# Optimization experiments

Hardware: AMD Instinct MI355X
Metric: run time of the kernel (lower is better)

The kernel has to match this reference:

```python
import jax, jax.numpy as jnp
import numpy as np

H_IN, W_IN = 128, 128  # sensor grid; region=(1,1), stride=(1,1) -> one RF per pixel


def setup_inputs() -> dict:
    key = jax.random.key(0)
    k1, k2, k3, k4, k5, k6 = jax.random.split(key, 6)
    B, N, C, HID = 8, 2048, 16, 128
    s = 1.0 / np.sqrt(HID)
    features = jax.random.normal(k1, (B, N, C), dtype=jnp.float32)
    coords = jax.random.randint(k2, (B, N, 2), 0, 128, dtype=jnp.int32)  # (x, y)
    w_ih = jax.random.normal(k3, (4 * HID, C), dtype=jnp.float32) * s
    w_hh = jax.random.normal(k4, (4 * HID, HID), dtype=jnp.float32) * s
    b_ih = jax.random.normal(k5, (4 * HID,), dtype=jnp.float32) * s
    b_hh = jax.random.normal(k6, (4 * HID,), dtype=jnp.float32) * s
    return {"features": features, "coords": coords, "w_ih": w_ih,
            "w_hh": w_hh, "b_ih": b_ih, "b_hh": b_hh}


def reference(features, coords, w_ih, w_hh, b_ih, b_hh):
    """MatrixLSTM with 1x1 non-overlapping receptive fields.

    Events (time-ordered along axis 1) are routed to their pixel's RF; a shared
    LSTM is run over each RF's event sequence and the last output per RF is
    scattered into a dense [B, hidden, H, W] map (zeros where no events).
    Implemented as one lax.scan over events with per-RF (h, c) state.
    """
    B, N, C = features.shape
    HID = w_hh.shape[1]
    # coord2idx: raster order y * W + x  -> RF id per event, [B, N]
    rf = coords[:, :, 1].astype(jnp.int32) * W_IN + coords[:, :, 0].astype(jnp.int32)
    bidx = jnp.arange(B)
    bias = b_ih + b_hh

    def step(carry, inp):
        h_all, c_all = carry              # [B, num_rf, HID] each
        x_t, rf_t = inp                   # [B, C], [B]
        h_prev = h_all[bidx, rf_t]        # gather per-RF state, [B, HID]
        c_prev = c_all[bidx, rf_t]
        gates = x_t @ w_ih.T + h_prev @ w_hh.T + bias  # [B, 4*HID]
        i, f, g, o = jnp.split(gates, 4, axis=-1)       # torch LSTM gate order
        i = jax.nn.sigmoid(i)
        f = jax.nn.sigmoid(f)
        g = jnp.tanh(g)
        o = jax.nn.sigmoid(o)
        c_new = f * c_prev + i * g
        h_new = o * jnp.tanh(c_new)
        h_all = h_all.at[bidx, rf_t].set(h_new)        # scatter back
        c_all = c_all.at[bidx, rf_t].set(c_new)
        return (h_all, c_all), None

    h0 = jnp.zeros((B, H_IN * W_IN, HID), features.dtype)
    c0 = jnp.zeros_like(h0)
    (h_all, _), _ = jax.lax.scan(step, (h0, c0),
                                 (features.transpose(1, 0, 2), rf.T))
    # final h per RF == LSTM output at each RF's last event; zeros if no events
    return h_all.reshape(B, H_IN, W_IN, HID).transpose(0, 3, 1, 2)
```

## Files before the change

### kernel.cpp

```cpp
#include <hip/hip_runtime.h>
#include <hip/hip_bf16.h>
#include <math.h>

#define B 8
#define N 2048
#define C 16
#define HID 128
#define NRF 16384
#define MAXLEN 8
#define MAXCH 2048

typedef __attribute__((ext_vector_type(4))) float f32x4;

__device__ __forceinline__ float sigf(float x) { return 1.f / (1.f + expf(-x)); }

__global__ __launch_bounds__(1024) void k_pre(
    const int* __restrict__ coords, const float* __restrict__ w_ih,
    const float* __restrict__ w_hh, const float* __restrict__ b_ih,
    const float* __restrict__ b_hh, float* __restrict__ w_ih_T,
    float* __restrict__ w_hh_T, float* __restrict__ biassum,
    int* __restrict__ map, int* __restrict__ cnt, int* __restrict__ mcnt,
    int* __restrict__ chainpk, int* __restrict__ mlist,
    int* __restrict__ slots) {
    int tid = threadIdx.x;
    if (blockIdx.x < 8) {
        int bb = blockIdx.x;
        __shared__ int cnt_l[NRF];
        __shared__ int nch_l, nmul_l;
#pragma unroll
        for (int i = 0; i < 16; i++) cnt_l[tid + 1024 * i] = 0;
        if (tid == 0) { nch_l = 0; nmul_l = 0; }
#pragma unroll
        for (int i = 0; i < 16; i++) map[bb * NRF + tid + 1024 * i] = -1;
        __syncthreads();
        int n0 = tid, n1 = tid + 1024;
        int2 c0 = ((const int2*)coords)[bb * N + n0];
        int2 c1 = ((const int2*)coords)[bb * N + n1];
        int rf0 = c0.y * 128 + c0.x;
        int rf1 = c1.y * 128 + c1.x;
        int pos0 = atomicAdd(&cnt_l[rf0], 1);
        int pos1 = atomicAdd(&cnt_l[rf1], 1);
        if (pos0 < MAXLEN) slots[((size_t)bb * NRF + rf0) * MAXLEN + pos0] = n0;
        if (pos1 < MAXLEN) slots[((size_t)bb * NRF + rf1) * MAXLEN + pos1] = n1;
        __syncthreads();
#pragma unroll
        for (int e = 0; e < 2; e++) {
            int rf = e ? rf1 : rf0;
            int pos = e ? pos1 : pos0;
            if (pos == 0) {
                int j = atomicAdd(&nch_l, 1);
                int len = cnt_l[rf];
                if (len > MAXLEN) len = MAXLEN;
                map[bb * NRF + rf] = j;
                int* sl = slots + ((size_t)bb * NRF + rf) * MAXLEN;
                int ev[MAXLEN];
#pragma unroll
                for (int t = 0; t < MAXLEN; t++) {
                    int v = sl[t];
                    ev[t] = (t < len) ? v : 0x7fffffff;
                }
#pragma unroll
                for (int a = 0; a < MAXLEN; a++)
#pragma unroll
                    for (int q = 0; q < MAXLEN - 1; q++) {
                        int u = ev[q], v = ev[q + 1];
                        ev[q] = min(u, v);
                        ev[q + 1] = max(u, v);
                    }
                if (len >= 2) {
                    for (int t = 0; t < len; t++) sl[t] = ev[t];
                    int m = atomicAdd(&nmul_l, 1);
                    if (m < 1024) mlist[bb * 1024 + m] = j | (rf << 11);
                }
                chainpk[bb * MAXCH + j] = ev[0] | (len << 11);
            }
        }
        __syncthreads();
        if (tid == 0) {
            cnt[bb] = nch_l;
            mcnt[bb] = (nmul_l > 1024) ? 1024 : nmul_l;
        }
    } else {
        int i = (blockIdx.x - 8) * 1024 + tid;
        if (i < C * 512) {
            int c = i >> 9, j = i & 511;
            w_ih_T[i] = w_ih[j * C + c];
        }
        if (i < HID * 512) {
            int k = i >> 9, j = i & 511;
            w_hh_T[i] = w_hh[j * HID + k];
        }
        if (i < 512) biassum[i] = b_ih[i] + b_hh[i];
    }
}

__global__ __launch_bounds__(512) void k_main(
    const float* __restrict__ features, const float* __restrict__ w_ih_T,
    const float* __restrict__ w_hh_T, const float* __restrict__ biassum,
    const int* __restrict__ cnt, const int* __restrict__ chainpk,
    const int* __restrict__ mcnt, const int* __restrict__ mlist,
    const int* __restrict__ slots, float* __restrict__ hfin) {
    int tid = threadIdx.x;
    __shared__ float ls_w[C * 512];
    __shared__ float ls_b[512];
    __shared__ int l_pk[16];
    __shared__ float h_s[HID], c_s[HID], x_s[16], g_s[512];

    if (blockIdx.x < 1024) {
        int bb = blockIdx.x >> 7;
        int m0 = blockIdx.x & 127;
        int M = mcnt[bb];
        if (m0 >= M) return;
        float wi[16];
#pragma unroll
        for (int c2 = 0; c2 < 16; c2++) wi[c2] = w_ih_T[c2 * 512 + tid];
        float bs = biassum[tid];
        for (int m = m0; m < M; m += 128) {
            int e = mlist[bb * 1024 + m];
            int j = e & 2047, rf = e >> 11;
            size_t idx = (size_t)(bb * MAXCH + j);
            int len = chainpk[bb * MAXCH + j] >> 11;
            const int* sl = slots + ((size_t)bb * NRF + rf) * MAXLEN;
            if (tid < 16) x_s[tid] = features[((size_t)(bb * N + sl[0])) * C + tid];
            if (tid < 128) c_s[tid] = 0.f;
            __syncthreads();
            for (int t = 0; t < len; t++) {
                float a0 = bs, a1 = 0.f, a2 = 0.f, a3 = 0.f;
#pragma unroll
                for (int c2 = 0; c2 < 16; c2++) a0 += wi[c2] * x_s[c2];
                if (t > 0) {
#pragma unroll 8
                    for (int k = 0; k < 128; k += 4) {
                        a0 += w_hh_T[k * 512 + tid]       * h_s[k];
                        a1 += w_hh_T[(k + 1) * 512 + tid] * h_s[k + 1];
                        a2 += w_hh_T[(k + 2) * 512 + tid] * h_s[k + 2];
                        a3 += w_hh_T[(k + 3) * 512 + tid] * h_s[k + 3];
                    }
                }
                g_s[tid] = (a0 + a1) + (a2 + a3);
                __syncthreads();
                if (tid < 128) {
                    float ig = sigf(g_s[tid]);
                    float fg = sigf(g_s[tid + 128]);
                    float gg = tanhf(g_s[tid + 256]);
                    float og = sigf(g_s[tid + 384]);
                    float cn = fg * c_s[tid] + ig * gg;
                    c_s[tid] = cn;
                    h_s[tid] = og * tanhf(cn);
                }
                if (tid < 16 && t + 1 < len)
                    x_s[tid] = features[((size_t)(bb * N + sl[t + 1])) * C + tid];
                __syncthreads();
            }
            if (tid < 128) hfin[idx * HID + tid] = h_s[tid];
            __syncthreads();
        }
    } else {
        int b2 = blockIdx.x - 1024;
        int bb = b2 >> 7;
        int slot0 = (b2 & 127) * 16;
        int nc = cnt[bb];
        if (tid < 16) {
            int j = slot0 + tid;
            l_pk[tid] = (j < nc) ? chainpk[bb * MAXCH + j] : -1;
        }
        for (int i = tid; i < C * 128; i += 512)
            ((float4*)ls_w)[i] = ((const float4*)w_ih_T)[i];
        ls_b[tid] = biassum[tid];
        __syncthreads();
        int w = tid >> 6, lane = tid & 63;
        int pk[2];
        float f[2];
#pragma unroll
        for (int s2 = 0; s2 < 2; s2++) {
            pk[s2] = l_pk[w * 2 + s2];
            f[s2] = 0.f;
            if (pk[s2] >= 0 && (pk[s2] >> 11) == 1 && lane < 16)
                f[s2] = features[((size_t)(bb * N + (pk[s2] & 2047))) * C + lane];
        }
#pragma unroll
        for (int s2 = 0; s2 < 2; s2++) {
            if (pk[s2] < 0 || (pk[s2] >> 11) != 1) continue;
            float ai0 = ls_b[lane],       ai1 = ls_b[lane + 64];
            float ag0 = ls_b[lane + 256], ag1 = ls_b[lane + 320];
            float ao0 = ls_b[lane + 384], ao1 = ls_b[lane + 448];
#pragma unroll
            for (int c2 = 0; c2 < 16; c2++) {
                float xv = __shfl(f[s2], c2, 64);
                ai0 += ls_w[c2 * 512 + lane]       * xv;
                ai1 += ls_w[c2 * 512 + lane + 64]  * xv;
                ag0 += ls_w[c2 * 512 + lane + 256] * xv;
                ag1 += ls_w[c2 * 512 + lane + 320] * xv;
                ao0 += ls_w[c2 * 512 + lane + 384] * xv;
                ao1 += ls_w[c2 * 512 + lane + 448] * xv;
            }
            float c0 = sigf(ai0) * tanhf(ag0);
            float c1 = sigf(ai1) * tanhf(ag1);
            float h0 = sigf(ao0) * tanhf(c0);
            float h1 = sigf(ao1) * tanhf(c1);
            size_t idx = (size_t)(bb * MAXCH + slot0 + w * 2 + s2);
            hfin[idx * HID + lane] = h0;
            hfin[idx * HID + lane + 64] = h1;
        }
    }
}

__global__ __launch_bounds__(256) void k_scatter(
    const float* __restrict__ hfin, const int* __restrict__ map,
    float* __restrict__ out) {
    int b = blockIdx.x >> 7;
    int y = blockIdx.x & 127;
    int t = threadIdx.x;
    int xq = t & 31;
    int hg = t >> 5;
    const int4* mrow = (const int4*)(map + b * NRF + y * 128);
    int4 kk = mrow[xq];
    const float* hb = hfin + (size_t)b * MAXCH * HID + hg * 16;
    float vx[16], vy[16], vz[16], vw[16];
#pragma unroll
    for (int q = 0; q < 4; q++) {
        float4 a = make_float4(0.f, 0.f, 0.f, 0.f);
        if (kk.x >= 0) a = *(const float4*)(hb + (size_t)kk.x * HID + q * 4);
        vx[q * 4 + 0] = a.x; vx[q * 4 + 1] = a.y;
        vx[q * 4 + 2] = a.z; vx[q * 4 + 3] = a.w;
    }
#pragma unroll
    for (int q = 0; q < 4; q++) {
        float4 a = make_float4(0.f, 0.f, 0.f, 0.f);
        if (kk.y >= 0) a = *(const float4*)(hb + (size_t)kk.y * HID + q * 4);
        vy[q * 4 + 0] = a.x; vy[q * 4 + 1] = a.y;
        vy[q * 4 + 2] = a.z; vy[q * 4 + 3] = a.w;
    }
#pragma unroll
    for (int q = 0; q < 4; q++) {
        float4 a = make_float4(0.f, 0.f, 0.f, 0.f);
        if (kk.z >= 0) a = *(const float4*)(hb + (size_t)kk.z * HID + q * 4);
        vz[q * 4 + 0] = a.x; vz[q * 4 + 1] = a.y;
        vz[q * 4 + 2] = a.z; vz[q * 4 + 3] = a.w;
    }
#pragma unroll
    for (int q = 0; q < 4; q++) {
        float4 a = make_float4(0.f, 0.f, 0.f, 0.f);
        if (kk.w >= 0) a = *(const float4*)(hb + (size_t)kk.w * HID + q * 4);
        vw[q * 4 + 0] = a.x; vw[q * 4 + 1] = a.y;
        vw[q * 4 + 2] = a.z; vw[q * 4 + 3] = a.w;
    }
#pragma unroll
    for (int hh = 0; hh < 16; hh++) {
        int hid = hg * 16 + hh;
        f32x4 v = {vx[hh], vy[hh], vz[hh], vw[hh]};
        __builtin_nontemporal_store(
            v, (f32x4*)(out + ((((size_t)b * HID + hid) * 128 + y) * 128) + xq * 4));
    }
}

extern "C" void kernel_launch(void* const* d_in, const int* in_sizes, int n_in,
                              void* d_out, int out_size, void* d_ws, size_t ws_size,
                              hipStream_t stream) {
    const float* features = (const float*)d_in[0];
    const int*   coords   = (const int*)d_in[1];
    const float* w_ih     = (const float*)d_in[2];
    const float* w_hh     = (const float*)d_in[3];
    const float* b_ih     = (const float*)d_in[4];
    const float* b_hh     = (const float*)d_in[5];
    float* out = (float*)d_out;

    char* ws = (char*)d_ws;
    float* w_ih_T   = (float*)(ws + 0);
    float* w_hh_T   = (float*)(ws + 32768);
    float* biassum  = (float*)(ws + 294912);
    int*   map      = (int*)(ws + 296960);
    int*   cnt      = (int*)(ws + 821248);
    int*   mcnt     = (int*)(ws + 821312);
    int*   chainpk  = (int*)(ws + 821376);
    int*   mlist    = (int*)(ws + 886912);
    int*   slots    = (int*)(ws + 919680);
    float* hfin     = (float*)(ws + 5113984);

    k_pre<<<dim3(81), dim3(1024), 0, stream>>>(
        coords, w_ih, w_hh, b_ih, b_hh, w_ih_T, w_hh_T, biassum,
        map, cnt, mcnt, chainpk, mlist, slots);
    k_main<<<dim3(2048), dim3(512), 0, stream>>>(
        features, w_ih_T, w_hh_T, biassum, cnt, chainpk, mcnt, mlist,
        slots, hfin);
    k_scatter<<<dim3(B * 128), dim3(256), 0, stream>>>(hfin, map, out);
}
```

Before: 131.4 us.

## Fuse preprocess, LSTM and scatter into one persistent kernel with grid barriers

Replaces the three separate launches with one 256-block persistent kernel. Two flag-based grid barriers with alternating magic values separate the preprocessing, LSTM and scatter phases. Each thread in the multi-event chain loop now keeps its full w_hh column (128 floats) in registers instead of re-reading it from global memory every step. Per-RF counters are packed as 16-bit halves in LDS so one 512-thread block can hold them, and the union shared layout lets phases reuse the same LDS. This removes launch gaps and repeated weight traffic, but it depends on all blocks being co-resident, adds heavy register pressure, and cuts the scatter and LSTM phases to fewer blocks.

```diff
diff --git a/kernel.cpp b/kernel.cpp
--- a/kernel.cpp
+++ b/kernel.cpp
@@ -1,5 +1,4 @@
 #include <hip/hip_runtime.h>
-#include <hip/hip_bf16.h>
 #include <math.h>
 
 #define B 8
@@ -9,50 +8,87 @@
 #define NRF 16384
 #define MAXLEN 8
 #define MAXCH 2048
+#define NBLK 256
+
+#define MAGIC1 0x1357BD13
+#define MAGIC2 0x2468ACE2
 
 typedef __attribute__((ext_vector_type(4))) float f32x4;
 
 __device__ __forceinline__ float sigf(float x) { return 1.f / (1.f + expf(-x)); }
 
-__global__ __launch_bounds__(1024) void k_pre(
-    const int* __restrict__ coords, const float* __restrict__ w_ih,
-    const float* __restrict__ w_hh, const float* __restrict__ b_ih,
-    const float* __restrict__ b_hh, float* __restrict__ w_ih_T,
-    float* __restrict__ w_hh_T, float* __restrict__ biassum,
-    int* __restrict__ map, int* __restrict__ cnt, int* __restrict__ mcnt,
+__device__ __forceinline__ void gridbar(int* flags, int magic) {
+    __syncthreads();
+    if (threadIdx.x == 0) {
+        __threadfence();
+        __hip_atomic_store(&flags[blockIdx.x], magic, __ATOMIC_RELEASE,
+                           __HIP_MEMORY_SCOPE_AGENT);
+    }
+    if (threadIdx.x < NBLK) {
+        while (__hip_atomic_load(&flags[threadIdx.x], __ATOMIC_ACQUIRE,
+                                 __HIP_MEMORY_SCOPE_AGENT) != magic)
+            __builtin_amdgcn_s_sleep(1);
+    }
+    __syncthreads();
+    __threadfence();
+}
+
+struct SmemPre {
+    unsigned int cnt16[NRF / 2];
+    int nch, nmul;
+};
+struct SmemMain {
+    float ls_w[C * 512];
+    float ls_b[512];
+    int   l_pk[64];
+    float h_s[HID], c_s[HID], x_s[16], g_s[512];
+};
+union Smem { SmemPre pre; SmemMain mn; };
+
+__global__ __launch_bounds__(512, 2) void k_all(
+    const float* __restrict__ features, const int* __restrict__ coords,
+    const float* __restrict__ w_ih, const float* __restrict__ w_hh,
+    const float* __restrict__ b_ih, const float* __restrict__ b_hh,
+    float* __restrict__ w_ih_T, float* __restrict__ w_hh_T,
+    float* __restrict__ biassum, int* __restrict__ map,
+    int* __restrict__ cnt, int* __restrict__ mcnt,
     int* __restrict__ chainpk, int* __restrict__ mlist,
-    int* __restrict__ slots) {
+    int* __restrict__ slots, float* __restrict__ hfin,
+    float* __restrict__ out, int* __restrict__ flags) {
+    __shared__ Smem sm;
     int tid = threadIdx.x;
-    if (blockIdx.x < 8) {
-        int bb = blockIdx.x;
-        __shared__ int cnt_l[NRF];
-        __shared__ int nch_l, nmul_l;
-#pragma unroll
-        for (int i = 0; i < 16; i++) cnt_l[tid + 1024 * i] = 0;
-        if (tid == 0) { nch_l = 0; nmul_l = 0; }
-#pragma unroll
-        for (int i = 0; i < 16; i++) map[bb * NRF + tid + 1024 * i] = -1;
+    int bid = blockIdx.x;
+
+    if (bid < 8) {
+        int bb = bid;
+#pragma unroll
+        for (int i = 0; i < 16; i++) sm.pre.cnt16[tid + 512 * i] = 0;
+        if (tid == 0) { sm.pre.nch = 0; sm.pre.nmul = 0; }
+#pragma unroll
+        for (int i = 0; i < 32; i++) map[bb * NRF + tid + 512 * i] = -1;
         __syncthreads();
-        int n0 = tid, n1 = tid + 1024;
-        int2 c0 = ((const int2*)coords)[bb * N + n0];
-        int2 c1 = ((const int2*)coords)[bb * N + n1];
-        int rf0 = c0.y * 128 + c0.x;
-        int rf1 = c1.y * 128 + c1.x;
-        int pos0 = atomicAdd(&cnt_l[rf0], 1);
-        int pos1 = atomicAdd(&cnt_l[rf1], 1);
-        if (pos0 < MAXLEN) slots[((size_t)bb * NRF + rf0) * MAXLEN + pos0] = n0;
-        if (pos1 < MAXLEN) slots[((size_t)bb * NRF + rf1) * MAXLEN + pos1] = n1;
+        int rf[4], pos[4];
+#pragma unroll
+        for (int e = 0; e < 4; e++) {
+            int n = tid + 512 * e;
+            int2 cc = ((const int2*)coords)[bb * N + n];
+            rf[e] = cc.y * 128 + cc.x;
+            int word = rf[e] >> 1, sh = (rf[e] & 1) << 4;
+            unsigned int old = atomicAdd(&sm.pre.cnt16[word], 1u << sh);
+            pos[e] = (int)((old >> sh) & 0xFFFFu);
+            if (pos[e] < MAXLEN)
+                slots[((size_t)bb * NRF + rf[e]) * MAXLEN + pos[e]] = n;
+        }
         __syncthreads();
 #pragma unroll
-        for (int e = 0; e < 2; e++) {
-            int rf = e ? rf1 : rf0;
-            int pos = e ? pos1 : pos0;
-            if (pos == 0) {
-                int j = atomicAdd(&nch_l, 1);
-                int len = cnt_l[rf];
+        for (int e = 0; e < 4; e++) {
+            if (pos[e] == 0) {
+                int j = atomicAdd(&sm.pre.nch, 1);
+                int word = rf[e] >> 1, sh = (rf[e] & 1) << 4;
+                int len = (int)((sm.pre.cnt16[word] >> sh) & 0xFFFFu);
                 if (len > MAXLEN) len = MAXLEN;
-                map[bb * NRF + rf] = j;
-                int* sl = slots + ((size_t)bb * NRF + rf) * MAXLEN;
+                map[bb * NRF + rf[e]] = j;
+                int* sl = slots + ((size_t)bb * NRF + rf[e]) * MAXLEN;
                 int ev[MAXLEN];
 #pragma unroll
                 for (int t = 0; t < MAXLEN; t++) {
@@ -69,22 +105,22 @@
                     }
                 if (len >= 2) {
                     for (int t = 0; t < len; t++) sl[t] = ev[t];
-                    int m = atomicAdd(&nmul_l, 1);
-                    if (m < 1024) mlist[bb * 1024 + m] = j | (rf << 11);
+                    int m = atomicAdd(&sm.pre.nmul, 1);
+                    if (m < 1024) mlist[bb * 1024 + m] = j | (rf[e] << 11);
                 }
                 chainpk[bb * MAXCH + j] = ev[0] | (len << 11);
             }
         }
         __syncthreads();
         if (tid == 0) {
-            cnt[bb] = nch_l;
-            mcnt[bb] = (nmul_l > 1024) ? 1024 : nmul_l;
+            cnt[bb] = sm.pre.nch;
+            mcnt[bb] = (sm.pre.nmul > 1024) ? 1024 : sm.pre.nmul;
         }
     } else {
-        int i = (blockIdx.x - 8) * 1024 + tid;
+        int i = (bid - 8) * 512 + tid;
         if (i < C * 512) {
-            int c = i >> 9, j = i & 511;
-            w_ih_T[i] = w_ih[j * C + c];
+            int c2 = i >> 9, j = i & 511;
+            w_ih_T[i] = w_ih[j * C + c2];
         }
         if (i < HID * 512) {
             int k = i >> 9, j = i & 511;
@@ -92,165 +128,152 @@
         }
         if (i < 512) biassum[i] = b_ih[i] + b_hh[i];
     }
-}
-
-__global__ __launch_bounds__(512) void k_main(
-    const float* __restrict__ features, const float* __restrict__ w_ih_T,
-    const float* __restrict__ w_hh_T, const float* __restrict__ biassum,
-    const int* __restrict__ cnt, const int* __restrict__ chainpk,
-    const int* __restrict__ mcnt, const int* __restrict__ mlist,
-    const int* __restrict__ slots, float* __restrict__ hfin) {
-    int tid = threadIdx.x;
-    __shared__ float ls_w[C * 512];
-    __shared__ float ls_b[512];
-    __shared__ int l_pk[16];
-    __shared__ float h_s[HID], c_s[HID], x_s[16], g_s[512];
-
-    if (blockIdx.x < 1024) {
-        int bb = blockIdx.x >> 7;
-        int m0 = blockIdx.x & 127;
+    gridbar(flags, MAGIC1);
+
+    {
+        for (int i = tid; i < C * 128; i += 512)
+            ((float4*)sm.mn.ls_w)[i] = ((const float4*)w_ih_T)[i];
+        sm.mn.ls_b[tid] = biassum[tid];
+        int gbb = bid >> 5;
+        int slot0 = (bid & 31) * 64;
+        if (tid < 64) {
+            int j = slot0 + tid;
+            sm.mn.l_pk[tid] = (j < cnt[gbb]) ? chainpk[gbb * MAXCH + j] : -1;
+        }
+
+        int bb = bid & 7, m0 = bid >> 3;
         int M = mcnt[bb];
-        if (m0 >= M) return;
+        float bs = biassum[tid];
         float wi[16];
-#pragma unroll
-        for (int c2 = 0; c2 < 16; c2++) wi[c2] = w_ih_T[c2 * 512 + tid];
-        float bs = biassum[tid];
-        for (int m = m0; m < M; m += 128) {
+        float wcol[128];
+        if (m0 < M) {
+#pragma unroll
+            for (int c2 = 0; c2 < 16; c2++) wi[c2] = w_ih_T[c2 * 512 + tid];
+#pragma unroll
+            for (int k = 0; k < 128; k++) wcol[k] = w_hh_T[k * 512 + tid];
+        }
+        for (int m = m0; m < M; m += 32) {
             int e = mlist[bb * 1024 + m];
             int j = e & 2047, rf = e >> 11;
             size_t idx = (size_t)(bb * MAXCH + j);
             int len = chainpk[bb * MAXCH + j] >> 11;
             const int* sl = slots + ((size_t)bb * NRF + rf) * MAXLEN;
-            if (tid < 16) x_s[tid] = features[((size_t)(bb * N + sl[0])) * C + tid];
-            if (tid < 128) c_s[tid] = 0.f;
+            if (tid < 16) sm.mn.x_s[tid] =
+                features[((size_t)(bb * N + sl[0])) * C + tid];
+            if (tid < 128) sm.mn.c_s[tid] = 0.f;
             __syncthreads();
             for (int t = 0; t < len; t++) {
                 float a0 = bs, a1 = 0.f, a2 = 0.f, a3 = 0.f;
 #pragma unroll
-                for (int c2 = 0; c2 < 16; c2++) a0 += wi[c2] * x_s[c2];
+                for (int c2 = 0; c2 < 16; c2++) a0 += wi[c2] * sm.mn.x_s[c2];
                 if (t > 0) {
-#pragma unroll 8
+#pragma unroll
                     for (int k = 0; k < 128; k += 4) {
-                        a0 += w_hh_T[k * 512 + tid]       * h_s[k];
-                        a1 += w_hh_T[(k + 1) * 512 + tid] * h_s[k + 1];
-                        a2 += w_hh_T[(k + 2) * 512 + tid] * h_s[k + 2];
-                        a3 += w_hh_T[(k + 3) * 512 + tid] * h_s[k + 3];
+                        a0 += wcol[k]     * sm.mn.h_s[k];
+                        a1 += wcol[k + 1] * sm.mn.h_s[k + 1];
+                        a2 += wcol[k + 2] * sm.mn.h_s[k + 2];
+                        a3 += wcol[k + 3] * sm.mn.h_s[k + 3];
                     }
                 }
-                g_s[tid] = (a0 + a1) + (a2 + a3);
+                sm.mn.g_s[tid] = (a0 + a1) + (a2 + a3);
                 __syncthreads();
                 if (tid < 128) {
-                    float ig = sigf(g_s[tid]);
-                    float fg = sigf(g_s[tid + 128]);
-                    float gg = tanhf(g_s[tid + 256]);
-                    float og = sigf(g_s[tid + 384]);
-                    float cn = fg * c_s[tid] + ig * gg;
-                    c_s[tid] = cn;
-                    h_s[tid] = og * tanhf(cn);
+                    float ig = sigf(sm.mn.g_s[tid]);
+                    float fg = sigf(sm.mn.g_s[tid + 128]);
+                    float gg = tanhf(sm.mn.g_s[tid + 256]);
+                    float og = sigf(sm.mn.g_s[tid + 384]);
+                    float cn = fg * sm.mn.c_s[tid] + ig * gg;
+                    sm.mn.c_s[tid] = cn;
+                    sm.mn.h_s[tid] = og * tanhf(cn);
                 }
                 if (tid < 16 && t + 1 < len)
-                    x_s[tid] = features[((size_t)(bb * N + sl[t + 1])) * C + tid];
+                    sm.mn.x_s[tid] =
+                        features[((size_t)(bb * N + sl[t + 1])) * C + tid];
                 __syncthreads();
             }
-            if (tid < 128) hfin[idx * HID + tid] = h_s[tid];
+            if (tid < 128) hfin[idx * HID + tid] = sm.mn.h_s[tid];
             __syncthreads();
         }
-    } else {
-        int b2 = blockIdx.x - 1024;
-        int bb = b2 >> 7;
-        int slot0 = (b2 & 127) * 16;
-        int nc = cnt[bb];
-        if (tid < 16) {
-            int j = slot0 + tid;
-            l_pk[tid] = (j < nc) ? chainpk[bb * MAXCH + j] : -1;
-        }
-        for (int i = tid; i < C * 128; i += 512)
-            ((float4*)ls_w)[i] = ((const float4*)w_ih_T)[i];
-        ls_b[tid] = biassum[tid];
         __syncthreads();
+
         int w = tid >> 6, lane = tid & 63;
-        int pk[2];
-        float f[2];
-#pragma unroll
-        for (int s2 = 0; s2 < 2; s2++) {
-            pk[s2] = l_pk[w * 2 + s2];
+        int pk[8];
+        float f[8];
+#pragma unroll
+        for (int s2 = 0; s2 < 8; s2++) {
+            pk[s2] = sm.mn.l_pk[w * 8 + s2];
             f[s2] = 0.f;
             if (pk[s2] >= 0 && (pk[s2] >> 11) == 1 && lane < 16)
-                f[s2] = features[((size_t)(bb * N + (pk[s2] & 2047))) * C + lane];
-        }
-#pragma unroll
-        for (int s2 = 0; s2 < 2; s2++) {
+                f[s2] = features[((size_t)(gbb * N + (pk[s2] & 2047))) * C + lane];
+        }
+#pragma unroll
+        for (int s2 = 0; s2 < 8; s2++) {
             if (pk[s2] < 0 || (pk[s2] >> 11) != 1) continue;
-            float ai0 = ls_b[lane],       ai1 = ls_b[lane + 64];
-            float ag0 = ls_b[lane + 256], ag1 = ls_b[lane + 320];
-            float ao0 = ls_b[lane + 384], ao1 = ls_b[lane + 448];
+            float ai0 = sm.mn.ls_b[lane],       ai1 = sm.mn.ls_b[lane + 64];
+            float ag0 = sm.mn.ls_b[lane + 256], ag1 = sm.mn.ls_b[lane + 320];
+            float ao0 = sm.mn.ls_b[lane + 384], ao1 = sm.mn.ls_b[lane + 448];
 #pragma unroll
             for (int c2 = 0; c2 < 16; c2++) {
                 float xv = __shfl(f[s2], c2, 64);
-                ai0 += ls_w[c2 * 512 + lane]       * xv;
-                ai1 += ls_w[c2 * 512 + lane + 64]  * xv;
-                ag0 += ls_w[c2 * 512 + lane + 256] * xv;
-                ag1 += ls_w[c2 * 512 + lane + 320] * xv;
-                ao0 += ls_w[c2 * 512 + lane + 384] * xv;
-                ao1 += ls_w[c2 * 512 + lane + 448] * xv;
-            }
-            float c0 = sigf(ai0) * tanhf(ag0);
-            float c1 = sigf(ai1) * tanhf(ag1);
-            float h0 = sigf(ao0) * tanhf(c0);
-            float h1 = sigf(ao1) * tanhf(c1);
-            size_t idx = (size_t)(bb * MAXCH + slot0 + w * 2 + s2);
+                ai0 += sm.mn.ls_w[c2 * 512 + lane]       * xv;
+                ai1 += sm.mn.ls_w[c2 * 512 + lane + 64]  * xv;
+                ag0 += sm.mn.ls_w[c2 * 512 + lane + 256] * xv;
+                ag1 += sm.mn.ls_w[c2 * 512 + lane + 320] * xv;
+                ao0 += sm.mn.ls_w[c2 * 512 + lane + 384] * xv;
+                ao1 += sm.mn.ls_w[c2 * 512 + lane + 448] * xv;
+            }
+            float cc0 = sigf(ai0) * tanhf(ag0);
+            float cc1 = sigf(ai1) * tanhf(ag1);
+            float h0 = sigf(ao0) * tanhf(cc0);
+            float h1 = sigf(ao1) * tanhf(cc1);
+            size_t idx = (size_t)(gbb * MAXCH + slot0 + w * 8 + s2);
             hfin[idx * HID + lane] = h0;
             hfin[idx * HID + lane + 64] = h1;
         }
     }
-}
-
-__global__ __launch_bounds__(256) void k_scatter(
-    const float* __restrict__ hfin, const int* __restrict__ map,
-    float* __restrict__ out) {
-    int b = blockIdx.x >> 7;
-    int y = blockIdx.x & 127;
-    int t = threadIdx.x;
-    int xq = t & 31;
-    int hg = t >> 5;
-    const int4* mrow = (const int4*)(map + b * NRF + y * 128);
-    int4 kk = mrow[xq];
-    const float* hb = hfin + (size_t)b * MAXCH * HID + hg * 16;
-    float vx[16], vy[16], vz[16], vw[16];
-#pragma unroll
-    for (int q = 0; q < 4; q++) {
-        float4 a = make_float4(0.f, 0.f, 0.f, 0.f);
-        if (kk.x >= 0) a = *(const float4*)(hb + (size_t)kk.x * HID + q * 4);
-        vx[q * 4 + 0] = a.x; vx[q * 4 + 1] = a.y;
-        vx[q * 4 + 2] = a.z; vx[q * 4 + 3] = a.w;
-    }
-#pragma unroll
-    for (int q = 0; q < 4; q++) {
-        float4 a = make_float4(0.f, 0.f, 0.f, 0.f);
-        if (kk.y >= 0) a = *(const float4*)(hb + (size_t)kk.y * HID + q * 4);
-        vy[q * 4 + 0] = a.x; vy[q * 4 + 1] = a.y;
-        vy[q * 4 + 2] = a.z; vy[q * 4 + 3] = a.w;
-    }
-#pragma unroll
-    for (int q = 0; q < 4; q++) {
-        float4 a = make_float4(0.f, 0.f, 0.f, 0.f);
-        if (kk.z >= 0) a = *(const float4*)(hb + (size_t)kk.z * HID + q * 4);
-        vz[q * 4 + 0] = a.x; vz[q * 4 + 1] = a.y;
-        vz[q * 4 + 2] = a.z; vz[q * 4 + 3] = a.w;
-    }
-#pragma unroll
-    for (int q = 0; q < 4; q++) {
-        float4 a = make_float4(0.f, 0.f, 0.f, 0.f);
-        if (kk.w >= 0) a = *(const float4*)(hb + (size_t)kk.w * HID + q * 4);
-        vw[q * 4 + 0] = a.x; vw[q * 4 + 1] = a.y;
-        vw[q * 4 + 2] = a.z; vw[q * 4 + 3] = a.w;
-    }
-#pragma unroll
-    for (int hh = 0; hh < 16; hh++) {
-        int hid = hg * 16 + hh;
-        f32x4 v = {vx[hh], vy[hh], vz[hh], vw[hh]};
-        __builtin_nontemporal_store(
-            v, (f32x4*)(out + ((((size_t)b * HID + hid) * 128 + y) * 128) + xq * 4));
+    gridbar(flags, MAGIC2);
+
+    {
+        int half = tid >> 8;
+        int t = tid & 255;
+        int xq = t & 31;
+        int hg = t >> 5;
+#pragma unroll
+        for (int p2 = 0; p2 < 2; p2++) {
+            int row = bid * 4 + p2 * 2 + half;
+            int b = row >> 7, y = row & 127;
+            const int4* mrow = (const int4*)(map + b * NRF + y * 128);
+            int4 kk = mrow[xq];
+            const float* hb = hfin + (size_t)b * MAXCH * HID + hg * 16;
+            float vx[16], vy[16], vz[16], vw[16];
+#pragma unroll
+            for (int q = 0; q < 4; q++) {
+                float4 a = make_float4(0.f, 0.f, 0.f, 0.f);
+                if (kk.x >= 0) a = *(const float4*)(hb + (size_t)kk.x * HID + q * 4);
+                vx[q * 4 + 0] = a.x; vx[q * 4 + 1] = a.y;
+                vx[q * 4 + 2] = a.z; vx[q * 4 + 3] = a.w;
+                a = make_float4(0.f, 0.f, 0.f, 0.f);
+                if (kk.y >= 0) a = *(const float4*)(hb + (size_t)kk.y * HID + q * 4);
+                vy[q * 4 + 0] = a.x; vy[q * 4 + 1] = a.y;
+                vy[q * 4 + 2] = a.z; vy[q * 4 + 3] = a.w;
+                a = make_float4(0.f, 0.f, 0.f, 0.f);
+                if (kk.z >= 0) a = *(const float4*)(hb + (size_t)kk.z * HID + q * 4);
+                vz[q * 4 + 0] = a.x; vz[q * 4 + 1] = a.y;
+                vz[q * 4 + 2] = a.z; vz[q * 4 + 3] = a.w;
+                a = make_float4(0.f, 0.f, 0.f, 0.f);
+                if (kk.w >= 0) a = *(const float4*)(hb + (size_t)kk.w * HID + q * 4);
+                vw[q * 4 + 0] = a.x; vw[q * 4 + 1] = a.y;
+                vw[q * 4 + 2] = a.z; vw[q * 4 + 3] = a.w;
+            }
+#pragma unroll
+            for (int hh = 0; hh < 16; hh++) {
+                int hid = hg * 16 + hh;
+                f32x4 v = {vx[hh], vy[hh], vz[hh], vw[hh]};
+                __builtin_nontemporal_store(
+                    v, (f32x4*)(out + ((((size_t)b * HID + hid) * 128 + y) * 128)
+                                + xq * 4));
+            }
+        }
     }
 }
 
@@ -276,12 +299,9 @@
     int*   mlist    = (int*)(ws + 886912);
     int*   slots    = (int*)(ws + 919680);
     float* hfin     = (float*)(ws + 5113984);
-
-    k_pre<<<dim3(81), dim3(1024), 0, stream>>>(
-        coords, w_ih, w_hh, b_ih, b_hh, w_ih_T, w_hh_T, biassum,
-        map, cnt, mcnt, chainpk, mlist, slots);
-    k_main<<<dim3(2048), dim3(512), 0, stream>>>(
-        features, w_ih_T, w_hh_T, biassum, cnt, chainpk, mcnt, mlist,
-        slots, hfin);
-    k_scatter<<<dim3(B * 128), dim3(256), 0, stream>>>(hfin, map, out);
+    int*   flags    = (int*)(ws + 13502592);
+
+    k_all<<<dim3(NBLK), dim3(512), 0, stream>>>(
+        features, coords, w_ih, w_hh, b_ih, b_hh, w_ih_T, w_hh_T, biassum,
+        map, cnt, mcnt, chainpk, mlist, slots, hfin, out, flags);
 }
```

After: 297.0 us. +126.0%, slower.
